# Performance work log

Hardware: AMD Instinct MI355X
Metric: run time of the kernel (lower is better)

Reference implementation:

```python
import jax, jax.numpy as jnp
import numpy as np

B, H, S, D = 4, 16, 2048, 64

def setup_inputs() -> dict:
    key = jax.random.key(0)
    kq, kk, kv, km = jax.random.split(key, 4)
    encodings_q = jax.random.normal(kq, (B, H, S, D), dtype=jnp.float32)
    encodings_k = jax.random.normal(kk, (B, H, S, D), dtype=jnp.float32)
    encodings_v = jax.random.normal(kv, (B, H, S, D), dtype=jnp.float32)
    mask = jax.random.randint(km, (B, 1, S, S), 0, 2).astype(jnp.bool_)
    return {"encodings_q": encodings_q, "encodings_k": encodings_k,
            "encodings_v": encodings_v, "mask": mask}

def reference(encodings_q, encodings_k, encodings_v, mask):
    # scaled dot-product attention: softmax(QK^T / sqrt(d) + mask) V
    d = encodings_q.shape[-1]
    scale = 1.0 / jnp.sqrt(jnp.asarray(d, dtype=encodings_q.dtype))
    # [B,H,S,S]
    scores = jnp.einsum('bhqd,bhkd->bhqk', encodings_q, encodings_k) * scale
    neg_inf = jnp.asarray(-1e9, dtype=scores.dtype)
    scores = jnp.where(mask, scores, neg_inf)  # True = keep, False = mask out
    attn = jax.nn.softmax(scores, axis=-1)
    out = jnp.einsum('bhqk,bhkd->bhqd', attn, encodings_v)
    return out
```

## Files before the change

kernel.cpp:

```cpp
#include <hip/hip_runtime.h>
#include <hip/hip_bf16.h>

#define B_ 4
#define H_ 16
#define S_ 2048
#define D_ 64
#define KBLK 32
#define NT (S_/KBLK)

typedef __attribute__((ext_vector_type(16))) float f32x16;
typedef __attribute__((ext_vector_type(4)))  unsigned int u32x4;
typedef __attribute__((ext_vector_type(8)))  short s16x8;
typedef __attribute__((ext_vector_type(8)))  __bf16 bf16x8;
typedef unsigned int u32;

__device__ __forceinline__ unsigned short f2bf(float f) {
    u32 u = __builtin_bit_cast(u32, f);
    u += 0x7FFFu + ((u >> 16) & 1u);
    return (unsigned short)(u >> 16);
}
__device__ __forceinline__ s16x8 cvt8(float4 a, float4 b) {
    s16x8 f;
    f[0] = (short)f2bf(a.x); f[1] = (short)f2bf(a.y);
    f[2] = (short)f2bf(a.z); f[3] = (short)f2bf(a.w);
    f[4] = (short)f2bf(b.x); f[5] = (short)f2bf(b.y);
    f[6] = (short)f2bf(b.z); f[7] = (short)f2bf(b.w);
    return f;
}
__device__ __forceinline__ f32x16 mfma32(s16x8 a, s16x8 b, f32x16 c) {
    return __builtin_amdgcn_mfma_f32_32x32x16_bf16(
        __builtin_bit_cast(bf16x8, a), __builtin_bit_cast(bf16x8, b), c, 0, 0, 0);
}
__device__ __forceinline__ void gll16(const void* g, void* l) {
    __builtin_amdgcn_global_load_lds(
        (const __attribute__((address_space(1))) unsigned int*)g,
        (__attribute__((address_space(3))) unsigned int*)l, 16, 0, 0);
}
__device__ __forceinline__ u32 pkcvt(float lo, float hi) {
    u32 r;
    asm("v_cvt_pk_bf16_f32 %0, %1, %2" : "=v"(r) : "v"(lo), "v"(hi));
    return r;
}
__device__ __forceinline__ float fand(float x, u32 m) {
    return __builtin_bit_cast(float, __builtin_bit_cast(u32, x) & m);
}

__global__ __launch_bounds__(256) void prep_kv(const float* __restrict__ K,
                                               const float* __restrict__ V,
                                               short* __restrict__ Kb,
                                               short* __restrict__ VT) {
    __shared__ float tile[64][65];
    const int bh = blockIdx.y;
    const int kc = blockIdx.x * 64;
    const int t = threadIdx.x;

    {
        const int r = t >> 2, c = (t & 3) * 16;
        const float* src = K + ((size_t)bh * S_ + kc + r) * D_ + c;
        float4 a0 = *(const float4*)(src + 0);
        float4 a1 = *(const float4*)(src + 4);
        float4 a2 = *(const float4*)(src + 8);
        float4 a3 = *(const float4*)(src + 12);
        short* dst = Kb + ((size_t)bh * S_ + kc + r) * D_ + c;
        *(s16x8*)dst       = cvt8(a0, a1);
        *(s16x8*)(dst + 8) = cvt8(a2, a3);
    }

    const float* src = V + (size_t)bh * S_ * D_ + (size_t)kc * D_;
#pragma unroll
    for (int p = 0; p < 4; ++p) {
        int idx = p * 256 + t;
        int r = idx >> 4;
        int c = (idx & 15) * 4;
        float4 v = *(const float4*)(src + (size_t)r * D_ + c);
        tile[r][c+0] = v.x; tile[r][c+1] = v.y; tile[r][c+2] = v.z; tile[r][c+3] = v.w;
    }
    __syncthreads();
    const int d = t >> 2, c0 = (t & 3) * 16;
    s16x8 o0, o1;
#pragma unroll
    for (int j = 0; j < 8; ++j) {
        o0[j] = (short)f2bf(tile[c0 + j][d]);
        o1[j] = (short)f2bf(tile[c0 + 8 + j][d]);
    }
    short* dst = VT + (size_t)bh * D_ * S_ + (size_t)d * S_ + kc + c0;
    *(s16x8*)dst = o0;
    *(s16x8*)(dst + 8) = o1;
}

__global__ __launch_bounds__(256) void mk_pairs(const int* __restrict__ M,
                                                u32* __restrict__ PM) {
    const u32 gid = blockIdx.x * 256 + threadIdx.x;
    const int w = gid & 7;
    const int q = (gid >> 3) & 2047;
    const int t = (gid >> 14) & 63;
    const int b = gid >> 20;
    const int k = t * 32 + 8 * (w & 3) + 4 * (w >> 2);

    const int4 a = *(const int4*)(M + (((size_t)b * S_ + q) * S_ + k));
    PM[gid] = (a.x ? 0xFFu : 0u) | (a.y ? 0xFF00u : 0u) |
              (a.z ? 0xFF0000u : 0u) | (a.w ? 0xFF000000u : 0u);
}

__global__ __launch_bounds__(128) void attn_fwd(
    const float* __restrict__ Q, const short* __restrict__ Kb,
    const short* __restrict__ VTb, const u32* __restrict__ PM,
    float* __restrict__ O)
{
    __shared__ short kbuf[2][KBLK * D_];
    __shared__ short vbuf[2][D_ * KBLK];

    const int tid = threadIdx.x;
    const int w  = tid >> 6;
    const int l  = tid & 63;
    const int ql = l & 31;
    const int h  = l >> 5;

    const int dd    = blockIdx.x;
    const int xcd   = dd & 7;
    const int slot  = dd >> 3;
    const int bh    = xcd * 8 + (slot >> 5);
    const int qtile = slot & 31;
    const int b     = bh >> 4;
    const int qrow  = qtile * 64 + w * 32 + ql;

    const float* Qp  = Q   + (size_t)bh * S_ * D_;
    const short* Kp  = Kb  + (size_t)bh * S_ * D_;
    const short* Vp  = VTb + (size_t)bh * D_ * S_;
    const u32*   pmp = PM  + (((size_t)b * NT) * S_ + qrow) * 8 + h * 4;
    float* Op = O + (size_t)bh * S_ * D_;

    const float qscale = 0.125f * 1.44269504088896f;
    s16x8 qfrag[4];
#pragma unroll
    for (int ks = 0; ks < 4; ++ks) {
        const float* src = Qp + (size_t)qrow * D_ + ks * 16 + h * 8;
        float4 a = *(const float4*)(src);
        float4 c = *(const float4*)(src + 4);
        float4 as = make_float4(a.x*qscale, a.y*qscale, a.z*qscale, a.w*qscale);
        float4 cs = make_float4(c.x*qscale, c.y*qscale, c.z*qscale, c.w*qscale);
        qfrag[ks] = cvt8(as, cs);
    }

    int offsK[4];
#pragma unroll
    for (int ks = 0; ks < 4; ++ks)
        offsK[ks] = ql * 128 + (((ks * 2 + h) ^ (ql & 7)) << 4);
    int offsV[2][2];
#pragma unroll
    for (int dt = 0; dt < 2; ++dt)
#pragma unroll
        for (int ks = 0; ks < 2; ++ks)
            offsV[dt][ks] = (dt * 32 + ql) * 64 + (((ks * 2 + h) ^ (ql & 3)) << 4);

    const int srowK = tid >> 3;
    const int sgK   = (tid & 7) ^ (srowK & 7);
    const char* KsrcB = (const char*)Kp + (size_t)srowK * 128 + sgK * 16;
    const int srowV = tid >> 2;
    const int sgV   = (tid & 3) ^ (srowV & 3);
    const char* VsrcB = (const char*)Vp + (size_t)srowV * (S_ * 2) + sgV * 16;

    f32x16 oacc0 = (f32x16)(0.f), oacc1 = (f32x16)(0.f);
    float lh = 0.f;

    {
        short* kd = &kbuf[0][w * 512];
        gll16(KsrcB,                       kd);
        gll16(KsrcB + 16 * 128,            kd + 1024);
        short* vd = &vbuf[0][w * 512];
        gll16(VsrcB,                       vd);
        gll16(VsrcB + (size_t)32 * S_ * 2, vd + 1024);
    }
    u32x4 bmn = *(const u32x4*)(pmp);

    for (int t = 0; t < NT; ++t) {
        const int cur = t & 1;
        asm volatile("s_waitcnt vmcnt(0)" ::: "memory");
        __syncthreads();

        const u32x4 bmc = bmn;

        const char* kbp = (const char*)kbuf[cur];
        f32x16 s0 = (f32x16)(0.f);
#pragma unroll
        for (int ks = 0; ks < 4; ++ks)
            s0 = mfma32(*(const s16x8*)(kbp + offsK[ks]), qfrag[ks], s0);

        if (t + 1 < NT) {
            short* kd = &kbuf[cur ^ 1][w * 512];
            const char* ks2 = KsrcB + (size_t)(t + 1) * (KBLK * 128);
            gll16(ks2,            kd);
            gll16(ks2 + 16 * 128, kd + 1024);
            short* vd = &vbuf[cur ^ 1][w * 512];
            const char* vs2 = VsrcB + (size_t)(t + 1) * (KBLK * 2);
            gll16(vs2,                       vd);
            gll16(vs2 + (size_t)32 * S_ * 2, vd + 1024);
            bmn = *(const u32x4*)(pmp + (size_t)(t + 1) * (S_ * 8));
        }

        float ps = 0.f;
        u32 pk0[8];
#pragma unroll
        for (int j = 0; j < 8; ++j) {
            const u32 word = bmc[j >> 1];
            const u32 mlo = (j & 1) ? (u32)(((int)(word <<  8)) >> 24)
                                    : (u32)(((int)(word << 24)) >> 24);
            const u32 mhi = (j & 1) ? (u32)(((int)word) >> 24)
                                    : (u32)(((int)(word << 16)) >> 24);
            float a0 = fand(__builtin_amdgcn_exp2f(s0[2*j]),   mlo);
            float a1 = fand(__builtin_amdgcn_exp2f(s0[2*j+1]), mhi);
            ps += a0 + a1;
            pk0[j] = pkcvt(a0, a1);
        }
        lh += ps;

        asm("v_permlane32_swap_b32 %0, %1" : "+v"(pk0[0]), "+v"(pk0[2]));
        asm("v_permlane32_swap_b32 %0, %1" : "+v"(pk0[1]), "+v"(pk0[3]));
        asm("v_permlane32_swap_b32 %0, %1" : "+v"(pk0[4]), "+v"(pk0[6]));
        asm("v_permlane32_swap_b32 %0, %1" : "+v"(pk0[5]), "+v"(pk0[7]));

        s16x8 pfrag[2];
        {
            u32x4 f0 = {pk0[0], pk0[1], pk0[2], pk0[3]};
            u32x4 f1 = {pk0[4], pk0[5], pk0[6], pk0[7]};
            pfrag[0] = __builtin_bit_cast(s16x8, f0);
            pfrag[1] = __builtin_bit_cast(s16x8, f1);
        }

        const char* vbp = (const char*)vbuf[cur];
#pragma unroll
        for (int ks = 0; ks < 2; ++ks) {
            oacc0 = mfma32(*(const s16x8*)(vbp + offsV[0][ks]), pfrag[ks], oacc0);
            oacc1 = mfma32(*(const s16x8*)(vbp + offsV[1][ks]), pfrag[ks], oacc1);
        }
    }

    lh += __shfl_xor(lh, 32);
    const float inv = 1.0f / lh;
#pragma unroll
    for (int rg = 0; rg < 4; ++rg) {
        float4 st;
        st.x = oacc0[rg*4+0] * inv; st.y = oacc0[rg*4+1] * inv;
        st.z = oacc0[rg*4+2] * inv; st.w = oacc0[rg*4+3] * inv;
        *(float4*)(Op + (size_t)qrow * D_ + rg * 8 + h * 4) = st;
        float4 su;
        su.x = oacc1[rg*4+0] * inv; su.y = oacc1[rg*4+1] * inv;
        su.z = oacc1[rg*4+2] * inv; su.w = oacc1[rg*4+3] * inv;
        *(float4*)(Op + (size_t)qrow * D_ + 32 + rg * 8 + h * 4) = su;
    }
}

extern "C" void kernel_launch(void* const* d_in, const int* in_sizes, int n_in,
                              void* d_out, int out_size, void* d_ws, size_t ws_size,
                              hipStream_t stream) {
    const float* Q = (const float*)d_in[0];
    const float* K = (const float*)d_in[1];
    const float* V = (const float*)d_in[2];
    const int*   M = (const int*)d_in[3];
    float* O = (float*)d_out;
    (void)in_sizes; (void)n_in; (void)out_size; (void)ws_size;

    char* ws = (char*)d_ws;
    short* Kb  = (short*)(ws);
    short* VTb = (short*)(ws + 16777216);
    u32*   PM  = (u32*)  (ws + 33554432);

    prep_kv <<<dim3(S_ / 64, B_ * H_), 256, 0, stream>>>(K, V, Kb, VTb);
    mk_pairs<<<16384, 256, 0, stream>>>(M, PM);
    attn_fwd<<<2048, 128, 0, stream>>>(Q, Kb, VTb, PM, O);
}
```

Measured before the change: 149.5 us.

## Give each wave private double-buffered K/V LDS tiles and drop block barriers

```diff
diff --git a/kernel.cpp b/kernel.cpp
--- a/kernel.cpp
+++ b/kernel.cpp
@@ -102,13 +102,13 @@
               (a.z ? 0xFF0000u : 0u) | (a.w ? 0xFF000000u : 0u);
 }
 
-__global__ __launch_bounds__(128) void attn_fwd(
+__global__ __launch_bounds__(256) void attn_fwd(
     const float* __restrict__ Q, const short* __restrict__ Kb,
     const short* __restrict__ VTb, const u32* __restrict__ PM,
     float* __restrict__ O)
 {
-    __shared__ short kbuf[2][KBLK * D_];
-    __shared__ short vbuf[2][D_ * KBLK];
+    __shared__ short kbuf[4][2][KBLK * D_ / 2 * 2];
+    __shared__ short vbuf[4][2][KBLK * D_ / 2 * 2];
 
     const int tid = threadIdx.x;
     const int w  = tid >> 6;
@@ -119,10 +119,10 @@
     const int dd    = blockIdx.x;
     const int xcd   = dd & 7;
     const int slot  = dd >> 3;
-    const int bh    = xcd * 8 + (slot >> 5);
-    const int qtile = slot & 31;
+    const int bh    = xcd * 8 + (slot >> 4);
+    const int qtile = slot & 15;
     const int b     = bh >> 4;
-    const int qrow  = qtile * 64 + w * 32 + ql;
+    const int qrow  = qtile * 128 + w * 32 + ql;
 
     const float* Qp  = Q   + (size_t)bh * S_ * D_;
     const short* Kp  = Kb  + (size_t)bh * S_ * D_;
@@ -151,50 +151,62 @@
     for (int dt = 0; dt < 2; ++dt)
 #pragma unroll
         for (int ks = 0; ks < 2; ++ks)
-            offsV[dt][ks] = (dt * 32 + ql) * 64 + (((ks * 2 + h) ^ (ql & 3)) << 4);
-
-    const int srowK = tid >> 3;
-    const int sgK   = (tid & 7) ^ (srowK & 7);
-    const char* KsrcB = (const char*)Kp + (size_t)srowK * 128 + sgK * 16;
-    const int srowV = tid >> 2;
-    const int sgV   = (tid & 3) ^ (srowV & 3);
-    const char* VsrcB = (const char*)Vp + (size_t)srowV * (S_ * 2) + sgV * 16;
+            offsV[dt][ks] = ql * 128 + (((dt * 4 + ks * 2 + h) ^ (ql & 7)) << 4);
+
+    const char* KsrcP[4];
+    const char* VsrcP[4];
+#pragma unroll
+    for (int pass = 0; pass < 4; ++pass) {
+        const int slot = pass * 64 + l;
+        const int r  = slot >> 3, p = slot & 7;
+        const int g  = p ^ (r & 7);
+        KsrcP[pass] = (const char*)Kp + (size_t)r * 128 + g * 16;
+        const int idx = p ^ (r & 7);
+        const int dt = idx >> 2, gk = idx & 3;
+        VsrcP[pass] = (const char*)Vp + (size_t)(dt * 32 + r) * (S_ * 2) + gk * 16;
+    }
+
+    short* kb0 = &kbuf[w][0][0];
+    short* kb1 = &kbuf[w][1][0];
+    short* vb0 = &vbuf[w][0][0];
+    short* vb1 = &vbuf[w][1][0];
 
     f32x16 oacc0 = (f32x16)(0.f), oacc1 = (f32x16)(0.f);
     float lh = 0.f;
 
-    {
-        short* kd = &kbuf[0][w * 512];
-        gll16(KsrcB,                       kd);
-        gll16(KsrcB + 16 * 128,            kd + 1024);
-        short* vd = &vbuf[0][w * 512];
-        gll16(VsrcB,                       vd);
-        gll16(VsrcB + (size_t)32 * S_ * 2, vd + 1024);
-    }
+#pragma unroll
+    for (int pass = 0; pass < 4; ++pass)
+        gll16(KsrcP[pass], kb0 + pass * 512);
+#pragma unroll
+    for (int pass = 0; pass < 4; ++pass)
+        gll16(VsrcP[pass], vb0 + pass * 512);
     u32x4 bmn = *(const u32x4*)(pmp);
 
     for (int t = 0; t < NT; ++t) {
         const int cur = t & 1;
         asm volatile("s_waitcnt vmcnt(0)" ::: "memory");
-        __syncthreads();
+        __builtin_amdgcn_sched_barrier(0);
 
         const u32x4 bmc = bmn;
-
-        const char* kbp = (const char*)kbuf[cur];
+        const char* kbp = (const char*)(cur ? kb1 : kb0);
+        const char* vbp = (const char*)(cur ? vb1 : vb0);
+
         f32x16 s0 = (f32x16)(0.f);
 #pragma unroll
         for (int ks = 0; ks < 4; ++ks)
             s0 = mfma32(*(const s16x8*)(kbp + offsK[ks]), qfrag[ks], s0);
 
         if (t + 1 < NT) {
-            short* kd = &kbuf[cur ^ 1][w * 512];
-            const char* ks2 = KsrcB + (size_t)(t + 1) * (KBLK * 128);
-            gll16(ks2,            kd);
-            gll16(ks2 + 16 * 128, kd + 1024);
-            short* vd = &vbuf[cur ^ 1][w * 512];
-            const char* vs2 = VsrcB + (size_t)(t + 1) * (KBLK * 2);
-            gll16(vs2,                       vd);
-            gll16(vs2 + (size_t)32 * S_ * 2, vd + 1024);
+            short* kd = cur ? kb0 : kb1;
+            short* vd = cur ? vb0 : vb1;
+            const size_t koff = (size_t)(t + 1) * (KBLK * 128);
+            const size_t voff = (size_t)(t + 1) * 64;
+#pragma unroll
+            for (int pass = 0; pass < 4; ++pass)
+                gll16(KsrcP[pass] + koff, kd + pass * 512);
+#pragma unroll
+            for (int pass = 0; pass < 4; ++pass)
+                gll16(VsrcP[pass] + voff, vd + pass * 512);
             bmn = *(const u32x4*)(pmp + (size_t)(t + 1) * (S_ * 8));
         }
 
@@ -227,7 +239,6 @@
             pfrag[1] = __builtin_bit_cast(s16x8, f1);
         }
 
-        const char* vbp = (const char*)vbuf[cur];
 #pragma unroll
         for (int ks = 0; ks < 2; ++ks) {
             oacc0 = mfma32(*(const s16x8*)(vbp + offsV[0][ks]), pfrag[ks], oacc0);
@@ -267,5 +278,5 @@
 
     prep_kv <<<dim3(S_ / 64, B_ * H_), 256, 0, stream>>>(K, V, Kb, VTb);
     mk_pairs<<<16384, 256, 0, stream>>>(M, PM);
-    attn_fwd<<<2048, 128, 0, stream>>>(Q, Kb, VTb, PM, O);
-}
+    attn_fwd<<<1024, 256, 0, stream>>>(Q, Kb, VTb, PM, O);
+}
```

New measurement: 146.1 us. 1.02x faster.
